# Optimization experiments

Hardware: AMD Instinct MI355X
Metric: run time of the kernel (lower is better)

The kernel has to match this reference:

```python
import jax, jax.numpy as jnp
import numpy as np

# dims: batch, nodes(sensors), window, embed, topk, MLP inter width
B, NODE, WIN, EMB, TOPK, INTER = 256, 512, 64, 64, 16, 512
NEG = 0.2      # LeakyReLU negative slope in GAT attention
EPS = 1e-5     # BatchNorm eps
N = B * NODE   # total graph nodes
E = N * TOPK   # total edges


def _bn(x, gamma, beta, axes):
    # training-mode BatchNorm: batch statistics (biased var), affine gamma/beta
    m = jnp.mean(x, axis=axes, keepdims=True)
    v = jnp.var(x, axis=axes, keepdims=True)
    return (x - m) * jax.lax.rsqrt(v + EPS) * gamma + beta


def setup_inputs() -> dict:
    key = jax.random.key(0)
    ks = jax.random.split(key, 12)
    sd = lambda k, shp, s: jax.random.normal(k, shp, jnp.float32) * s
    return {
        "data": jax.random.normal(ks[0], (B, NODE, WIN), jnp.float32),
        "org_edge_index": jax.random.randint(ks[1], (2, NODE), 0, NODE, dtype=jnp.int32),  # unused by forward
        "W_emb": sd(ks[2], (NODE, EMB), 0.1),          # nn.Embedding weight
        "W_lin": sd(ks[3], (EMB, WIN), 0.1),           # GraphLayer.lin (no bias)
        "att_i": sd(ks[4], (EMB,), 0.1),
        "att_j": sd(ks[5], (EMB,), 0.1),
        "att_em_i": sd(ks[6], (EMB,), 0.1),
        "att_em_j": sd(ks[7], (EMB,), 0.1),
        "b_gnn": jnp.zeros((EMB,), jnp.float32),       # GraphLayer bias
        "g_bn1": jnp.ones((EMB,), jnp.float32), "b_bn1": jnp.zeros((EMB,), jnp.float32),
        "g_bn2": jnp.ones((EMB,), jnp.float32), "b_bn2": jnp.zeros((EMB,), jnp.float32),
        "W1": sd(ks[8], (INTER, EMB), 0.05), "b1": jnp.zeros((INTER,), jnp.float32),
        "g_bn3": jnp.ones((INTER,), jnp.float32), "b_bn3": jnp.zeros((INTER,), jnp.float32),
        "W2": sd(ks[9], (1, INTER), 0.05), "b2": jnp.zeros((1,), jnp.float32),
    }


def reference(data, org_edge_index, W_emb, W_lin, att_i, att_j, att_em_i, att_em_j,
              b_gnn, g_bn1, b_bn1, g_bn2, b_bn2, W1, b1, g_bn3, b_bn3, W2, b2):
    x = data.reshape(N, WIN)

    # ---- graph structure learning: cosine-sim top-k on DETACHED embeddings ----
    w = jax.lax.stop_gradient(W_emb)
    nw = w * jax.lax.rsqrt(jnp.sum(w * w, axis=-1, keepdims=True))
    cos = nw @ nw.T                                  # [NODE, NODE]
    _, topk_idx = jax.lax.top_k(cos, TOPK)           # [NODE, TOPK]; diag==1 -> self in top-k,
                                                     # so remove+add self-loops is a no-op on the edge set
    offs = (jnp.arange(N // NODE) * NODE)[:, None]   # batch offsets
    src = (topk_idx.reshape(-1)[None, :] + offs).reshape(-1)                 # [E] source j
    dst = (jnp.repeat(jnp.arange(NODE), TOPK)[None, :] + offs).reshape(-1)   # [E] target i (sorted)

    # ---- GAT-style message passing (heads=1, concat=False) ----
    xl = x @ W_lin.T                                 # [N, EMB]
    # per-node attention scores for key = [Wx || embedding]
    s_i = xl @ att_i + jnp.tile(W_emb @ att_em_i, B)  # [N]
    s_j = xl @ att_j + jnp.tile(W_emb @ att_em_j, B)  # [N]
    alpha = s_i[dst] + s_j[src]                      # [E]
    alpha = jnp.where(alpha > 0, alpha, NEG * alpha)  # leaky_relu
    # segment softmax over edges grouped by target node
    amax = jax.ops.segment_max(alpha, dst, num_segments=N, indices_are_sorted=True)
    ex = jnp.exp(alpha - amax[dst])
    den = jax.ops.segment_sum(ex, dst, num_segments=N, indices_are_sorted=True)
    attw = ex / den[dst]                             # [E]
    agg = jax.ops.segment_sum(attw[:, None] * xl[src], dst,
                              num_segments=N, indices_are_sorted=True)  # [N, EMB]
    h = jax.nn.relu(_bn(agg + b_gnn, g_bn1, b_bn1, axes=0))             # GNNLayer bn+relu

    # ---- readout: mul by embedding, BN over channels, MLP head (dropout=eval/identity) ----
    z = h.reshape(B, NODE, EMB) * W_emb[None]        # [B, NODE, EMB]
    z = jax.nn.relu(_bn(z, g_bn2, b_bn2, axes=(0, 1)))
    z = jax.nn.relu(_bn(z @ W1.T + b1, g_bn3, b_bn3, axes=(0, 1)))      # [B, NODE, INTER]
    out = (z @ W2.T + b2).reshape(B, NODE)
    return out
```

## Files before the change

kernel.cpp:

```cpp
#include <hip/hip_runtime.h>
#include <hip/hip_bf16.h>

constexpr int BATCH = 256, NNODE = 512, WINW = 64, EMBD = 64, KTOP = 16, CIN = 512;
constexpr int NTOT = BATCH * NNODE;
constexpr float NEGS = 0.2f;
constexpr float EPSBN = 1e-5f;

typedef __attribute__((ext_vector_type(8))) short bf16x8;
typedef __attribute__((ext_vector_type(4))) float f32x4;

union U8 { uint4 u; bf16x8 b; };

__device__ inline float bf2f(unsigned u16) {
  union { unsigned u; float f; } v; v.u = u16 << 16; return v.f;
}
__device__ inline unsigned short f2bf(float x) {
  union { float f; unsigned u; } v; v.f = x;
  unsigned r = v.u + 0x7fff + ((v.u >> 16) & 1);
  return (unsigned short)(r >> 16);
}

__global__ void k_prep(const float* __restrict__ W_emb,
                       const float* __restrict__ att_em_i,
                       const float* __restrict__ att_em_j,
                       float* __restrict__ nw, float* __restrict__ emb_si,
                       float* __restrict__ emb_sj) {
  int i = blockIdx.x, e = threadIdx.x;
  float w  = W_emb[i * EMBD + e];
  float sq = w * w;
  float si = w * att_em_i[e];
  float sj = w * att_em_j[e];
  for (int o = 32; o > 0; o >>= 1) {
    sq += __shfl_xor(sq, o);
    si += __shfl_xor(si, o);
    sj += __shfl_xor(sj, o);
  }
  nw[i * EMBD + e] = w * rsqrtf(sq);
  if (e == 0) { emb_si[i] = si; emb_sj[i] = sj; }
}

__global__ __launch_bounds__(256) void k_topk(const float* __restrict__ nw,
                                              int* __restrict__ topk) {
  __shared__ float nwi[EMBD];
  __shared__ float wbv[4];
  __shared__ int   wbi[4];
  __shared__ int   winner;
  int i = blockIdx.x, t = threadIdx.x, wv = t >> 6, ln = t & 63;
  if (t < EMBD) nwi[t] = nw[i * EMBD + t];
  __syncthreads();
  float v0 = 0.f, v1 = 0.f;
  #pragma unroll
  for (int k = 0; k < EMBD; k++) {
    v0 += nw[t * EMBD + k] * nwi[k];
    v1 += nw[(t + 256) * EMBD + k] * nwi[k];
  }
  for (int sel = 0; sel < KTOP; sel++) {
    float bv; int bi;
    if (v1 > v0) { bv = v1; bi = t + 256; } else { bv = v0; bi = t; }
    #pragma unroll
    for (int o = 1; o < 64; o <<= 1) {
      float ov = __shfl_xor(bv, o);
      int   oi = __shfl_xor(bi, o);
      if (ov > bv || (ov == bv && oi < bi)) { bv = ov; bi = oi; }
    }
    if (ln == 0) { wbv[wv] = bv; wbi[wv] = bi; }
    __syncthreads();
    if (t == 0) {
      float B = wbv[0]; int I = wbi[0];
      #pragma unroll
      for (int w = 1; w < 4; w++)
        if (wbv[w] > B || (wbv[w] == B && wbi[w] < I)) { B = wbv[w]; I = wbi[w]; }
      topk[i * KTOP + sel] = I;
      winner = I;
    }
    __syncthreads();
    int wi = winner;
    if (wi == t) v0 = -3.f;
    else if (wi == t + 256) v1 = -3.f;
  }
}

__global__ __launch_bounds__(256) void k_xl(
    const float* __restrict__ data, const float* __restrict__ W_lin,
    const float* __restrict__ att_i, const float* __restrict__ att_j,
    const float* __restrict__ emb_si, const float* __restrict__ emb_sj,
    unsigned* __restrict__ xlb, float* __restrict__ s_i, float* __restrict__ s_j) {
  __shared__ unsigned short ht[4][16 * 72];
  const int t = threadIdx.x, w = t >> 6, ln = t & 63;
  const int lm = ln & 15, lq = ln >> 4, kb = lq * 8;

  bf16x8 bfrag[4][2];
  float ai4[4], aj4[4];
  #pragma unroll
  for (int ti = 0; ti < 4; ti++) {
    int ch = ti * 16 + lm;
    ai4[ti] = att_i[ch]; aj4[ti] = att_j[ch];
    #pragma unroll
    for (int s = 0; s < 2; s++) {
      const float* wp = W_lin + ch * WINW + s * 32 + kb;
      float4 w0 = *(const float4*)wp;
      float4 w1 = *(const float4*)(wp + 4);
      bf16x8 f;
      f[0] = (short)f2bf(w0.x); f[1] = (short)f2bf(w0.y);
      f[2] = (short)f2bf(w0.z); f[3] = (short)f2bf(w0.w);
      f[4] = (short)f2bf(w1.x); f[5] = (short)f2bf(w1.y);
      f[6] = (short)f2bf(w1.z); f[7] = (short)f2bf(w1.w);
      bfrag[ti][s] = f;
    }
  }
  uint4* xlb4 = (uint4*)xlb;
  const uint4* hp4 = (const uint4*)&ht[w][0];
  #pragma unroll
  for (int tt = 0; tt < 2; tt++) {
    int tile = blockIdx.x * 8 + w * 2 + tt;
    const float* dr = data + (size_t)(tile * 16 + lm) * WINW + kb;
    f32x4 acc[4];
    #pragma unroll
    for (int ti = 0; ti < 4; ti++) acc[ti] = (f32x4){0.f, 0.f, 0.f, 0.f};
    #pragma unroll
    for (int s = 0; s < 2; s++) {
      float4 d0 = *(const float4*)(dr + s * 32);
      float4 d1 = *(const float4*)(dr + s * 32 + 4);
      bf16x8 af;
      af[0] = (short)f2bf(d0.x); af[1] = (short)f2bf(d0.y);
      af[2] = (short)f2bf(d0.z); af[3] = (short)f2bf(d0.w);
      af[4] = (short)f2bf(d1.x); af[5] = (short)f2bf(d1.y);
      af[6] = (short)f2bf(d1.z); af[7] = (short)f2bf(d1.w);
      #pragma unroll
      for (int ti = 0; ti < 4; ti++)
        acc[ti] = __builtin_amdgcn_mfma_f32_16x16x32_bf16(af, bfrag[ti][s], acc[ti], 0, 0, 0);
    }
    #pragma unroll
    for (int r = 0; r < 4; r++) {
      int ndl = lq * 4 + r;
      int nd = tile * 16 + ndl;
      float si = 0.f, sj = 0.f;
      #pragma unroll
      for (int ti = 0; ti < 4; ti++) {
        float v = acc[ti][r];
        ht[w][ndl * 72 + ti * 16 + lm] = f2bf(v);
        si += v * ai4[ti];
        sj += v * aj4[ti];
      }
      si += __shfl_xor(si, 1); si += __shfl_xor(si, 2);
      si += __shfl_xor(si, 4); si += __shfl_xor(si, 8);
      sj += __shfl_xor(sj, 1); sj += __shfl_xor(sj, 2);
      sj += __shfl_xor(sj, 4); sj += __shfl_xor(sj, 8);
      if (lm == 0) {
        int node = nd & (NNODE - 1);
        s_i[nd] = si + emb_si[node];
        s_j[nd] = sj + emb_sj[node];
      }
    }
    #pragma unroll
    for (int g = 0; g < 2; g++) {
      int slot = g * 64 + ln;
      int row = slot >> 3, grp = slot & 7;
      xlb4[(size_t)(tile * 16 + row) * 8 + grp] = hp4[row * 9 + grp];
    }
  }
}

__global__ __launch_bounds__(256) void k_edge(
    const unsigned* __restrict__ xlb, const float* __restrict__ s_i,
    const float* __restrict__ s_j, const int* __restrict__ topk,
    unsigned* __restrict__ aggb, float* __restrict__ gsum1,
    float* __restrict__ gss1) {
  __shared__ float redb[4][128];
  const int t = threadIdx.x, w = t >> 6, ln = t & 63;
  const int nd4 = ln >> 4, l4 = ln & 15;
  const int b = blockIdx.x & 255;
  const int seg = blockIdx.x >> 8;
  const int boff = b * NNODE;
  const int nbase = seg * 64 + w * 16;
  const uint2* xl2 = (const uint2*)xlb;
  uint2* ag2 = (uint2*)aggb;
  float ps0 = 0.f, ps1 = 0.f, ps2 = 0.f, ps3 = 0.f;
  float qs0 = 0.f, qs1 = 0.f, qs2 = 0.f, qs3 = 0.f;
  for (int it = 0; it < 4; it++) {
    int nl = nbase + it * 4 + nd4;
    int n = boff + nl;
    const int4* tp = (const int4*)(topk + nl * KTOP);
    int4 i0 = tp[0], i1 = tp[1], i2 = tp[2], i3 = tp[3];
    int idx[16] = {i0.x, i0.y, i0.z, i0.w, i1.x, i1.y, i1.z, i1.w,
                   i2.x, i2.y, i2.z, i2.w, i3.x, i3.y, i3.z, i3.w};
    float sid = s_i[n];
    float al[16], mx = -1e30f;
    #pragma unroll
    for (int k = 0; k < KTOP; k++) {
      float a = sid + s_j[boff + idx[k]];
      a = a > 0.f ? a : NEGS * a;
      al[k] = a;
      mx = fmaxf(mx, a);
    }
    float den = 0.f;
    #pragma unroll
    for (int k = 0; k < KTOP; k++) { al[k] = __expf(al[k] - mx); den += al[k]; }
    float inv = 1.f / den;
    float ax = 0.f, ay = 0.f, az = 0.f, aw = 0.f;
    #pragma unroll
    for (int k = 0; k < KTOP; k++) {
      uint2 v = xl2[(size_t)(boff + idx[k]) * 16 + l4];
      ax += al[k] * bf2f(v.x & 0xffffu);
      ay += al[k] * bf2f(v.x >> 16);
      az += al[k] * bf2f(v.y & 0xffffu);
      aw += al[k] * bf2f(v.y >> 16);
    }
    ax *= inv; ay *= inv; az *= inv; aw *= inv;
    uint2 st;
    st.x = (unsigned)f2bf(ax) | ((unsigned)f2bf(ay) << 16);
    st.y = (unsigned)f2bf(az) | ((unsigned)f2bf(aw) << 16);
    ag2[(size_t)n * 16 + l4] = st;
    ps0 += ax; ps1 += ay; ps2 += az; ps3 += aw;
    qs0 += ax * ax; qs1 += ay * ay; qs2 += az * az; qs3 += aw * aw;
  }
  #pragma unroll
  for (int o = 16; o <= 32; o <<= 1) {
    ps0 += __shfl_xor(ps0, o); ps1 += __shfl_xor(ps1, o);
    ps2 += __shfl_xor(ps2, o); ps3 += __shfl_xor(ps3, o);
    qs0 += __shfl_xor(qs0, o); qs1 += __shfl_xor(qs1, o);
    qs2 += __shfl_xor(qs2, o); qs3 += __shfl_xor(qs3, o);
  }
  if (ln < 16) {
    float4 a = {ps0, ps1, ps2, ps3};
    float4 q = {qs0, qs1, qs2, qs3};
    *(float4*)&redb[w][ln * 4] = a;
    *(float4*)&redb[w][64 + ln * 4] = q;
  }
  __syncthreads();
  if (t < 64) {
    atomicAdd(&gsum1[t], redb[0][t] + redb[1][t] + redb[2][t] + redb[3][t]);
  } else if (t < 128) {
    int e = t - 64;
    atomicAdd(&gss1[e], redb[0][64 + e] + redb[1][64 + e] + redb[2][64 + e] + redb[3][64 + e]);
  }
}

__global__ void k_fin(const float* __restrict__ gsum, const float* __restrict__ gss,
                      const float* __restrict__ g, const float* __restrict__ bb,
                      float* __restrict__ a, float* __restrict__ c, int C) {
  int e = blockIdx.x * blockDim.x + threadIdx.x;
  if (e >= C) return;
  const float invn = 1.f / (float)NTOT;
  float m = gsum[e] * invn;
  float v = gss[e] * invn - m * m;
  float aa = g[e] * rsqrtf(v + EPSBN);
  a[e] = aa;
  c[e] = bb[e] - m * aa;
}

__global__ __launch_bounds__(256) void k_zstats3(
    const unsigned* __restrict__ aggb, const float* __restrict__ W_emb,
    const float* __restrict__ a1, const float* __restrict__ c1,
    float* __restrict__ gsum2, float* __restrict__ gss2) {
  __shared__ float red[4][8][32];
  int t = threadIdx.x;
  int gid = blockIdx.x * 256 + t;
  int p = t & 31;
  int c0 = 2 * p;
  float a10 = a1[c0], a11 = a1[c0 + 1], c10 = c1[c0], c11 = c1[c0 + 1];
  const float2* we2  = (const float2*)W_emb;
  float ps0 = 0.f, ps1 = 0.f, q0 = 0.f, q1 = 0.f;
  int stride = gridDim.x * 256;
  for (int idx = gid; idx < NTOT * 32; idx += stride) {
    unsigned u = aggb[idx];
    float vx = bf2f(u & 0xffffu), vy = bf2f(u >> 16);
    int node = (idx >> 5) & (NNODE - 1);
    float2 w = we2[node * 32 + p];
    float z0 = vx * a10 + c10; z0 = z0 > 0.f ? z0 : 0.f; z0 *= w.x;
    float z1 = vy * a11 + c11; z1 = z1 > 0.f ? z1 : 0.f; z1 *= w.y;
    ps0 += z0; q0 += z0 * z0; ps1 += z1; q1 += z1 * z1;
  }
  int g = t >> 5;
  red[0][g][p] = ps0; red[1][g][p] = ps1; red[2][g][p] = q0; red[3][g][p] = q1;
  __syncthreads();
  if (t < 128) {
    int v = t >> 5, p2 = t & 31;
    float s = 0.f;
    #pragma unroll
    for (int k = 0; k < 8; k++) s += red[v][k][p2];
    float* dst = (v & 2) ? gss2 : gsum2;
    atomicAdd(&dst[2 * p2 + (v & 1)], s);
  }
}

__global__ __launch_bounds__(256) void k_gram2(
    const unsigned* __restrict__ aggb, const float* __restrict__ W_emb,
    const float* __restrict__ a1, const float* __restrict__ c1,
    const float* __restrict__ a2, const float* __restrict__ c2,
    float* __restrict__ Gpart, float* __restrict__ hpart,
    unsigned* __restrict__ hb) {
  __shared__ float smem[4 * 4480];
  __shared__ float hred[4][64];
  const int t = threadIdx.x, wv = t >> 6, ln = t & 63;
  const int lm = ln & 15, lq = ln >> 4;
  const int r4 = ln & 7, ch8 = ln >> 3;
  const int c0 = ch8 * 8;
  float a1v[8], c1v[8], a2v[8], c2v[8];
  #pragma unroll
  for (int j = 0; j < 8; j++) {
    a1v[j] = a1[c0 + j]; c1v[j] = c1[c0 + j];
    a2v[j] = a2[c0 + j]; c2v[j] = c2[c0 + j];
  }
  unsigned* ht = (unsigned*)(smem + wv * 4480);
  bf16x8 ones;
  #pragma unroll
  for (int j = 0; j < 8; j++) ones[j] = (short)0x3F80;
  f32x4 acc[4][4];
  f32x4 accS[4];
  #pragma unroll
  for (int i = 0; i < 4; i++) {
    accS[i] = (f32x4){0.f, 0.f, 0.f, 0.f};
    #pragma unroll
    for (int j = 0; j < 4; j++) acc[i][j] = (f32x4){0.f, 0.f, 0.f, 0.f};
  }
  const uint4* ab4 = (const uint4*)aggb;
  uint4* hb4 = (uint4*)hb;
  const float4* we4 = (const float4*)W_emb;
  const int blockrow = blockIdx.x * 256;
  #pragma unroll
  for (int ck = 0; ck < 2; ck++) {
    int k0 = blockrow + wv * 64 + ck * 32;
    #pragma unroll
    for (int rr2 = 0; rr2 < 2; rr2++) {
      float h2[2][8];
      #pragma unroll
      for (int rh = 0; rh < 2; rh++) {
        int lr = r4 * 4 + rr2 * 2 + rh;
        int row = k0 + lr;
        int node = row & (NNODE - 1);
        uint4 u = ab4[(size_t)row * 8 + ch8];
        float4 w0 = we4[node * 16 + ch8 * 2];
        float4 w1 = we4[node * 16 + ch8 * 2 + 1];
        float gv[8] = {bf2f(u.x & 0xffffu), bf2f(u.x >> 16),
                       bf2f(u.y & 0xffffu), bf2f(u.y >> 16),
                       bf2f(u.z & 0xffffu), bf2f(u.z >> 16),
                       bf2f(u.w & 0xffffu), bf2f(u.w >> 16)};
        float wv8[8] = {w0.x, w0.y, w0.z, w0.w, w1.x, w1.y, w1.z, w1.w};
        uint hp[4];
        #pragma unroll
        for (int j = 0; j < 8; j++) {
          float z = gv[j] * a1v[j] + c1v[j];
          z = z > 0.f ? z : 0.f;
          z *= wv8[j];
          float hh = z * a2v[j] + c2v[j];
          hh = hh > 0.f ? hh : 0.f;
          h2[rh][j] = hh;
        }
        #pragma unroll
        for (int j = 0; j < 4; j++)
          hp[j] = (unsigned)f2bf(h2[rh][2 * j]) | ((unsigned)f2bf(h2[rh][2 * j + 1]) << 16);
        hb4[(size_t)row * 8 + ch8] = make_uint4(hp[0], hp[1], hp[2], hp[3]);
      }
      #pragma unroll
      for (int cc = 0; cc < 8; cc++) {
        int ch = c0 + cc;
        int base = ch * 20 + ((ch >> 3) & 3) * 4;
        ht[base + r4 * 2 + rr2] =
            (unsigned)f2bf(h2[0][cc]) | ((unsigned)f2bf(h2[1][cc]) << 16);
      }
    }
    bf16x8 frag[4];
    #pragma unroll
    for (int i = 0; i < 4; i++) {
      int ch = i * 16 + lm;
      int base = ch * 20 + ((ch >> 3) & 3) * 4;
      frag[i] = *(const bf16x8*)(ht + base + lq * 4);
    }
    #pragma unroll
    for (int i = 0; i < 4; i++) {
      #pragma unroll
      for (int j = 0; j < 4; j++)
        acc[i][j] = __builtin_amdgcn_mfma_f32_16x16x32_bf16(frag[i], frag[j], acc[i][j], 0, 0, 0);
      accS[i] = __builtin_amdgcn_mfma_f32_16x16x32_bf16(frag[i], ones, accS[i], 0, 0, 0);
    }
  }
  __syncthreads();
  float* Gb = smem + wv * 4480;
  #pragma unroll
  for (int i = 0; i < 4; i++) {
    #pragma unroll
    for (int j = 0; j < 4; j++) {
      float4 vv = {acc[i][j][0], acc[i][j][1], acc[i][j][2], acc[i][j][3]};
      *(float4*)(Gb + (j * 16 + lm) * 68 + i * 16 + lq * 4) = vv;
    }
    if (lm == 0) {
      float4 sv = {accS[i][0], accS[i][1], accS[i][2], accS[i][3]};
      *(float4*)&hred[wv][i * 16 + lq * 4] = sv;
    }
  }
  __syncthreads();
  for (int k = t; k < 4096; k += 256) {
    int col = k >> 6, row = k & 63;
    int o = col * 68 + row;
    Gpart[(size_t)blockIdx.x * 4096 + k] =
        smem[o] + smem[4480 + o] + smem[2 * 4480 + o] + smem[3 * 4480 + o];
  }
  if (t < 64)
    hpart[(size_t)blockIdx.x * 64 + t] =
        hred[0][t] + hred[1][t] + hred[2][t] + hred[3][t];
}

__global__ __launch_bounds__(256) void k_gred(const float* __restrict__ Gpart,
                                              const float* __restrict__ hpart,
                                              float* __restrict__ G,
                                              float* __restrict__ hsum) {
  int wi = blockIdx.x * 256 + threadIdx.x;
  if (wi < 32768) {
    int e = wi & 4095, seg = wi >> 12;
    float s = 0.f;
    #pragma unroll 8
    for (int k = 0; k < 64; k++) s += Gpart[(size_t)((seg << 6) + k) * 4096 + e];
    atomicAdd(&G[e], s);
  } else {
    int wi2 = wi - 32768;
    int e = wi2 & 63, seg = wi2 >> 6;
    float s = 0.f;
    #pragma unroll 8
    for (int k = 0; k < 64; k++) s += hpart[(size_t)((seg << 6) + k) * 64 + e];
    atomicAdd(&hsum[e], s);
  }
}

__global__ __launch_bounds__(64) void k_fin3q(
    const float* __restrict__ G, const float* __restrict__ hsum,
    const float* __restrict__ W1, const float* __restrict__ b1,
    const float* __restrict__ g3, const float* __restrict__ b3,
    float* __restrict__ a3, float* __restrict__ c3) {
  __shared__ float sw[64];
  int c = blockIdx.x, i = threadIdx.x;
  float w1i = W1[c * 64 + i];
  sw[i] = w1i;
  __syncthreads();
  float gw = 0.f;
  #pragma unroll
  for (int j = 0; j < 64; j++) gw += G[j * 64 + i] * sw[j];
  float t1 = w1i * gw;
  float t2 = w1i * hsum[i];
  for (int o = 32; o > 0; o >>= 1) { t1 += __shfl_xor(t1, o); t2 += __shfl_xor(t2, o); }
  if (i == 0) {
    float b1c = b1[c];
    const float fn = (float)NTOT, invn = 1.f / fn;
    float sum3 = t2 + fn * b1c;
    float ss3  = t1 + 2.f * b1c * t2 + fn * b1c * b1c;
    float m = sum3 * invn;
    float v = ss3 * invn - m * m;
    float aa = g3[c] * rsqrtf(v + EPSBN);
    a3[c] = aa;
    c3[c] = b3[c] - m * aa;
  }
}

__global__ __launch_bounds__(512) void k_gout3(
    const unsigned* __restrict__ hb, const float* __restrict__ W1,
    const float* __restrict__ b1, const float* __restrict__ a3,
    const float* __restrict__ c3, const float* __restrict__ W2,
    const float* __restrict__ b2, float* __restrict__ out) {
  const int t = threadIdx.x, wv = t >> 6, ln = t & 63;
  const int lm = ln & 15, lq = ln >> 4, kb = lq * 8;
  bf16x8 bfrag[4][2];
  float b1c[4], a3c[4], c3c[4], w2c[4];
  #pragma unroll
  for (int nt = 0; nt < 4; nt++) {
    int col = wv * 64 + nt * 16 + lm;
    b1c[nt] = b1[col]; a3c[nt] = a3[col]; c3c[nt] = c3[col]; w2c[nt] = W2[col];
    #pragma unroll
    for (int s = 0; s < 2; s++) {
      const float* wp = W1 + col * EMBD + s * 32 + kb;
      float4 w0 = *(const float4*)wp;
      float4 w1 = *(const float4*)(wp + 4);
      bf16x8 f;
      f[0] = (short)f2bf(w0.x); f[1] = (short)f2bf(w0.y);
      f[2] = (short)f2bf(w0.z); f[3] = (short)f2bf(w0.w);
      f[4] = (short)f2bf(w1.x); f[5] = (short)f2bf(w1.y);
      f[6] = (short)f2bf(w1.z); f[7] = (short)f2bf(w1.w);
      bfrag[nt][s] = f;
    }
  }
  float b2v = b2[0];
  const uint4* h4 = (const uint4*)hb;
  for (int tile = blockIdx.x; tile < NTOT / 16; tile += gridDim.x) {
    int rowbase = tile * 16;
    U8 ua, ub;
    ua.u = h4[(size_t)(rowbase + lm) * 8 + lq];
    ub.u = h4[(size_t)(rowbase + lm) * 8 + 4 + lq];
    f32x4 acc[4];
    #pragma unroll
    for (int nt = 0; nt < 4; nt++) acc[nt] = (f32x4){0.f, 0.f, 0.f, 0.f};
    #pragma unroll
    for (int nt = 0; nt < 4; nt++)
      acc[nt] = __builtin_amdgcn_mfma_f32_16x16x32_bf16(ua.b, bfrag[nt][0], acc[nt], 0, 0, 0);
    #pragma unroll
    for (int nt = 0; nt < 4; nt++)
      acc[nt] = __builtin_amdgcn_mfma_f32_16x16x32_bf16(ub.b, bfrag[nt][1], acc[nt], 0, 0, 0);
    #pragma unroll
    for (int r = 0; r < 4; r++) {
      float p = 0.f;
      #pragma unroll
      for (int nt = 0; nt < 4; nt++) {
        float z2 = acc[nt][r] + b1c[nt];
        float y = z2 * a3c[nt] + c3c[nt];
        y = y > 0.f ? y : 0.f;
        p += y * w2c[nt];
      }
      p += __shfl_xor(p, 1); p += __shfl_xor(p, 2);
      p += __shfl_xor(p, 4); p += __shfl_xor(p, 8);
      if (lm == 0) {
        if (wv == 0) p += b2v;
        atomicAdd(&out[rowbase + lq * 4 + r], p);
      }
    }
  }
}

extern "C" void kernel_launch(void* const* d_in, const int* in_sizes, int n_in,
                              void* d_out, int out_size, void* d_ws, size_t ws_size,
                              hipStream_t stream) {
  const float* data     = (const float*)d_in[0];
  const float* W_emb    = (const float*)d_in[2];
  const float* W_lin    = (const float*)d_in[3];
  const float* att_i    = (const float*)d_in[4];
  const float* att_j    = (const float*)d_in[5];
  const float* att_em_i = (const float*)d_in[6];
  const float* att_em_j = (const float*)d_in[7];
  const float* g_bn1    = (const float*)d_in[9];
  const float* b_bn1    = (const float*)d_in[10];
  const float* g_bn2    = (const float*)d_in[11];
  const float* b_bn2    = (const float*)d_in[12];
  const float* W1       = (const float*)d_in[13];
  const float* b1       = (const float*)d_in[14];
  const float* g_bn3    = (const float*)d_in[15];
  const float* b_bn3    = (const float*)d_in[16];
  const float* W2       = (const float*)d_in[17];
  const float* b2       = (const float*)d_in[18];
  float* out = (float*)d_out;

  char* p = (char*)d_ws;
  auto alloc = [&](size_t bytes) {
    void* r = (void*)p;
    p += (bytes + 255) & ~(size_t)255;
    return r;
  };
  unsigned* aggb  = (unsigned*)alloc((size_t)NTOT * EMBD * 2);
  unsigned* xlb   = (unsigned*)alloc((size_t)NTOT * EMBD * 2);
  unsigned* hb    = (unsigned*)alloc((size_t)NTOT * EMBD * 2);
  float*    Gpart = (float*)alloc((size_t)512 * 4096 * 4);
  float*    hpart = (float*)alloc((size_t)512 * 64 * 4);
  float*    s_i   = (float*)alloc((size_t)NTOT * 4);
  float*    s_j   = (float*)alloc((size_t)NTOT * 4);
  float*    nw    = (float*)alloc((size_t)NNODE * EMBD * 4);
  float*    emb_si = (float*)alloc(NNODE * 4);
  float*    emb_sj = (float*)alloc(NNODE * 4);
  int*      topk   = (int*)alloc(NNODE * KTOP * 4);
  float*    stats  = (float*)alloc(4416 * 4);
  float*    coefs  = (float*)alloc(1280 * 4);

  float* gsum1 = stats;       float* gss1 = stats + 64;
  float* gsum2 = stats + 128; float* gss2 = stats + 192;
  float* G     = stats + 256; float* hsum = stats + 4352;
  float* a1 = coefs;       float* c1 = coefs + 64;
  float* a2 = coefs + 128; float* c2 = coefs + 192;
  float* a3 = coefs + 256; float* c3 = coefs + 768;

  hipMemsetAsync(stats, 0, 4416 * 4, stream);
  hipMemsetAsync(out, 0, (size_t)NTOT * 4, stream);

  k_prep<<<NNODE, 64, 0, stream>>>(W_emb, att_em_i, att_em_j, nw, emb_si, emb_sj);
  k_topk<<<NNODE, 256, 0, stream>>>(nw, topk);
  k_xl<<<1024, 256, 0, stream>>>(data, W_lin, att_i, att_j, emb_si, emb_sj,
                                 xlb, s_i, s_j);
  k_edge<<<2048, 256, 0, stream>>>(xlb, s_i, s_j, topk, aggb, gsum1, gss1);
  k_fin<<<1, 64, 0, stream>>>(gsum1, gss1, g_bn1, b_bn1, a1, c1, EMBD);
  k_zstats3<<<1024, 256, 0, stream>>>(aggb, W_emb, a1, c1, gsum2, gss2);
  k_fin<<<1, 64, 0, stream>>>(gsum2, gss2, g_bn2, b_bn2, a2, c2, EMBD);
  k_gram2<<<512, 256, 0, stream>>>(aggb, W_emb, a1, c1, a2, c2, Gpart, hpart, hb);
  k_gred<<<130, 256, 0, stream>>>(Gpart, hpart, G, hsum);
  k_fin3q<<<CIN, 64, 0, stream>>>(G, hsum, W1, b1, g_bn3, b_bn3, a3, c3);
  k_gout3<<<512, 512, 0, stream>>>(hb, W1, b1, a3, c3, W2, b2, out);
}
```

Before: 309.5 us.

## Fuse linear projection and edge attention per batch graph in LDS

Merges the xl projection kernel and the edge-attention kernel into one kernel, with one 1024-thread block per batch graph. The projected features (bf16, XOR-swizzled) and attention scores stay in shared memory instead of going through global memory, which removes the xlb, s_i and s_j round trips and one launch. The cost is a large LDS footprint (about 72KB) and only 256 blocks, so occupancy and parallelism are lower, and there is a block-wide barrier between the GEMM phase and the gather phase.

```diff
diff --git a/kernel.cpp b/kernel.cpp
--- a/kernel.cpp
+++ b/kernel.cpp
@@ -80,12 +80,18 @@
   }
 }
 
-__global__ __launch_bounds__(256) void k_xl(
+__global__ __launch_bounds__(1024) void k_fuse2(
     const float* __restrict__ data, const float* __restrict__ W_lin,
     const float* __restrict__ att_i, const float* __restrict__ att_j,
     const float* __restrict__ emb_si, const float* __restrict__ emb_sj,
-    unsigned* __restrict__ xlb, float* __restrict__ s_i, float* __restrict__ s_j) {
-  __shared__ unsigned short ht[4][16 * 72];
+    const int* __restrict__ topk,
+    unsigned* __restrict__ aggb, float* __restrict__ gsum1,
+    float* __restrict__ gss1) {
+  __shared__ unsigned xlp[NNODE * 32];
+  __shared__ float ssi[NNODE];
+  __shared__ float ssj[NNODE];
+  __shared__ float redb[16 * 128];
+  const int b = blockIdx.x;
   const int t = threadIdx.x, w = t >> 6, ln = t & 63;
   const int lm = ln & 15, lq = ln >> 4, kb = lq * 8;
 
@@ -108,12 +114,10 @@
       bfrag[ti][s] = f;
     }
   }
-  uint4* xlb4 = (uint4*)xlb;
-  const uint4* hp4 = (const uint4*)&ht[w][0];
   #pragma unroll
   for (int tt = 0; tt < 2; tt++) {
-    int tile = blockIdx.x * 8 + w * 2 + tt;
-    const float* dr = data + (size_t)(tile * 16 + lm) * WINW + kb;
+    int tile = w * 2 + tt;
+    const float* dr = data + ((size_t)b * NNODE + tile * 16 + lm) * WINW + kb;
     f32x4 acc[4];
     #pragma unroll
     for (int ti = 0; ti < 4; ti++) acc[ti] = (f32x4){0.f, 0.f, 0.f, 0.f};
@@ -132,63 +136,42 @@
     }
     #pragma unroll
     for (int r = 0; r < 4; r++) {
-      int ndl = lq * 4 + r;
-      int nd = tile * 16 + ndl;
+      int nd = tile * 16 + lq * 4 + r;
+      int sw = ((nd >> 2) & 3) << 3;
       float si = 0.f, sj = 0.f;
       #pragma unroll
       for (int ti = 0; ti < 4; ti++) {
         float v = acc[ti][r];
-        ht[w][ndl * 72 + ti * 16 + lm] = f2bf(v);
+        float vo = __shfl_xor(v, 1);
         si += v * ai4[ti];
         sj += v * aj4[ti];
+        if (!(lm & 1)) {
+          unsigned u = (unsigned)f2bf(v) | ((unsigned)f2bf(vo) << 16);
+          xlp[nd * 32 + ((ti * 8 + (lm >> 1)) ^ sw)] = u;
+        }
       }
       si += __shfl_xor(si, 1); si += __shfl_xor(si, 2);
       si += __shfl_xor(si, 4); si += __shfl_xor(si, 8);
       sj += __shfl_xor(sj, 1); sj += __shfl_xor(sj, 2);
       sj += __shfl_xor(sj, 4); sj += __shfl_xor(sj, 8);
-      if (lm == 0) {
-        int node = nd & (NNODE - 1);
-        s_i[nd] = si + emb_si[node];
-        s_j[nd] = sj + emb_sj[node];
-      }
-    }
-    #pragma unroll
-    for (int g = 0; g < 2; g++) {
-      int slot = g * 64 + ln;
-      int row = slot >> 3, grp = slot & 7;
-      xlb4[(size_t)(tile * 16 + row) * 8 + grp] = hp4[row * 9 + grp];
-    }
-  }
-}
-
-__global__ __launch_bounds__(256) void k_edge(
-    const unsigned* __restrict__ xlb, const float* __restrict__ s_i,
-    const float* __restrict__ s_j, const int* __restrict__ topk,
-    unsigned* __restrict__ aggb, float* __restrict__ gsum1,
-    float* __restrict__ gss1) {
-  __shared__ float redb[4][128];
-  const int t = threadIdx.x, w = t >> 6, ln = t & 63;
+      if (lm == 0) { ssi[nd] = si + emb_si[nd]; ssj[nd] = sj + emb_sj[nd]; }
+    }
+  }
+  __syncthreads();
   const int nd4 = ln >> 4, l4 = ln & 15;
-  const int b = blockIdx.x & 255;
-  const int seg = blockIdx.x >> 8;
-  const int boff = b * NNODE;
-  const int nbase = seg * 64 + w * 16;
-  const uint2* xl2 = (const uint2*)xlb;
-  uint2* ag2 = (uint2*)aggb;
-  float ps0 = 0.f, ps1 = 0.f, ps2 = 0.f, ps3 = 0.f;
-  float qs0 = 0.f, qs1 = 0.f, qs2 = 0.f, qs3 = 0.f;
-  for (int it = 0; it < 4; it++) {
-    int nl = nbase + it * 4 + nd4;
-    int n = boff + nl;
-    const int4* tp = (const int4*)(topk + nl * KTOP);
+  float psx = 0.f, psy = 0.f, psz = 0.f, psw = 0.f;
+  float qsx = 0.f, qsy = 0.f, qsz = 0.f, qsw = 0.f;
+  for (int it = 0; it < 8; it++) {
+    int node = w * 32 + it * 4 + nd4;
+    const int4* tp = (const int4*)(topk + node * KTOP);
     int4 i0 = tp[0], i1 = tp[1], i2 = tp[2], i3 = tp[3];
     int idx[16] = {i0.x, i0.y, i0.z, i0.w, i1.x, i1.y, i1.z, i1.w,
                    i2.x, i2.y, i2.z, i2.w, i3.x, i3.y, i3.z, i3.w};
-    float sid = s_i[n];
+    float sid = ssi[node];
     float al[16], mx = -1e30f;
     #pragma unroll
     for (int k = 0; k < KTOP; k++) {
-      float a = sid + s_j[boff + idx[k]];
+      float a = sid + ssj[idx[k]];
       a = a > 0.f ? a : NEGS * a;
       al[k] = a;
       mx = fmaxf(mx, a);
@@ -200,7 +183,8 @@
     float ax = 0.f, ay = 0.f, az = 0.f, aw = 0.f;
     #pragma unroll
     for (int k = 0; k < KTOP; k++) {
-      uint2 v = xl2[(size_t)(boff + idx[k]) * 16 + l4];
+      int sw2 = ((idx[k] >> 2) & 3) << 2;
+      uint2 v = *(const uint2*)&xlp[idx[k] * 32 + 2 * (l4 ^ sw2)];
       ax += al[k] * bf2f(v.x & 0xffffu);
       ay += al[k] * bf2f(v.x >> 16);
       az += al[k] * bf2f(v.y & 0xffffu);
@@ -210,29 +194,35 @@
     uint2 st;
     st.x = (unsigned)f2bf(ax) | ((unsigned)f2bf(ay) << 16);
     st.y = (unsigned)f2bf(az) | ((unsigned)f2bf(aw) << 16);
-    ag2[(size_t)n * 16 + l4] = st;
-    ps0 += ax; ps1 += ay; ps2 += az; ps3 += aw;
-    qs0 += ax * ax; qs1 += ay * ay; qs2 += az * az; qs3 += aw * aw;
+    *(uint2*)(aggb + (((size_t)b * NNODE + node) << 5) + l4 * 2) = st;
+    psx += ax; psy += ay; psz += az; psw += aw;
+    qsx += ax * ax; qsy += ay * ay; qsz += az * az; qsw += aw * aw;
   }
   #pragma unroll
   for (int o = 16; o <= 32; o <<= 1) {
-    ps0 += __shfl_xor(ps0, o); ps1 += __shfl_xor(ps1, o);
-    ps2 += __shfl_xor(ps2, o); ps3 += __shfl_xor(ps3, o);
-    qs0 += __shfl_xor(qs0, o); qs1 += __shfl_xor(qs1, o);
-    qs2 += __shfl_xor(qs2, o); qs3 += __shfl_xor(qs3, o);
+    psx += __shfl_xor(psx, o); psy += __shfl_xor(psy, o);
+    psz += __shfl_xor(psz, o); psw += __shfl_xor(psw, o);
+    qsx += __shfl_xor(qsx, o); qsy += __shfl_xor(qsy, o);
+    qsz += __shfl_xor(qsz, o); qsw += __shfl_xor(qsw, o);
   }
   if (ln < 16) {
-    float4 a = {ps0, ps1, ps2, ps3};
-    float4 q = {qs0, qs1, qs2, qs3};
-    *(float4*)&redb[w][ln * 4] = a;
-    *(float4*)&redb[w][64 + ln * 4] = q;
+    float4 a = {psx, psy, psz, psw};
+    float4 q = {qsx, qsy, qsz, qsw};
+    *(float4*)&redb[w * 128 + ln * 4] = a;
+    *(float4*)&redb[w * 128 + 64 + ln * 4] = q;
   }
   __syncthreads();
   if (t < 64) {
-    atomicAdd(&gsum1[t], redb[0][t] + redb[1][t] + redb[2][t] + redb[3][t]);
+    float s = 0.f;
+    #pragma unroll
+    for (int w16 = 0; w16 < 16; w16++) s += redb[w16 * 128 + t];
+    atomicAdd(&gsum1[t], s);
   } else if (t < 128) {
     int e = t - 64;
-    atomicAdd(&gss1[e], redb[0][64 + e] + redb[1][64 + e] + redb[2][64 + e] + redb[3][64 + e]);
+    float s = 0.f;
+    #pragma unroll
+    for (int w16 = 0; w16 < 16; w16++) s += redb[w16 * 128 + 64 + e];
+    atomicAdd(&gss1[e], s);
   }
 }
 
@@ -542,12 +532,9 @@
     return r;
   };
   unsigned* aggb  = (unsigned*)alloc((size_t)NTOT * EMBD * 2);
-  unsigned* xlb   = (unsigned*)alloc((size_t)NTOT * EMBD * 2);
   unsigned* hb    = (unsigned*)alloc((size_t)NTOT * EMBD * 2);
   float*    Gpart = (float*)alloc((size_t)512 * 4096 * 4);
   float*    hpart = (float*)alloc((size_t)512 * 64 * 4);
-  float*    s_i   = (float*)alloc((size_t)NTOT * 4);
-  float*    s_j   = (float*)alloc((size_t)NTOT * 4);
   float*    nw    = (float*)alloc((size_t)NNODE * EMBD * 4);
   float*    emb_si = (float*)alloc(NNODE * 4);
   float*    emb_sj = (float*)alloc(NNODE * 4);
@@ -567,9 +554,8 @@
 
   k_prep<<<NNODE, 64, 0, stream>>>(W_emb, att_em_i, att_em_j, nw, emb_si, emb_sj);
   k_topk<<<NNODE, 256, 0, stream>>>(nw, topk);
-  k_xl<<<1024, 256, 0, stream>>>(data, W_lin, att_i, att_j, emb_si, emb_sj,
-                                 xlb, s_i, s_j);
-  k_edge<<<2048, 256, 0, stream>>>(xlb, s_i, s_j, topk, aggb, gsum1, gss1);
+  k_fuse2<<<BATCH, 1024, 0, stream>>>(data, W_lin, att_i, att_j, emb_si, emb_sj,
+                                      topk, aggb, gsum1, gss1);
   k_fin<<<1, 64, 0, stream>>>(gsum1, gss1, g_bn1, b_bn1, a1, c1, EMBD);
   k_zstats3<<<1024, 256, 0, stream>>>(aggb, W_emb, a1, c1, gsum2, gss2);
   k_fin<<<1, 64, 0, stream>>>(gsum2, gss2, g_bn2, b_bn2, a2, c2, EMBD);
```

Result: faster. 267.4 us (-13.6%).
